# Kernel tuning notes

Measured on AMD Instinct MI355X. Metric: run time of the kernel, lower is better.

The kernel has to match this reference:

```python
import jax, jax.numpy as jnp
import numpy as np

N_PTS = 10000
BATCH = 2048          # hypotheses per RANSAC iteration
MAX_ITER = 10
SAMPLE_SIZE = 4       # minimal sample for homography DLT
INL_TH = 2.0          # squared symmetric transfer error threshold
EPS = 1e-8


def normalize_points(pts):
    # kornia.geometry.normalize_points: center + isotropic scale to mean dist sqrt(2)
    mean = pts.mean(axis=1, keepdims=True)                       # [B,1,2]
    d = jnp.linalg.norm(pts - mean, axis=-1).mean(axis=-1)       # [B]
    s = jnp.sqrt(jnp.asarray(2.0, pts.dtype)) / (d + EPS)
    B = pts.shape[0]
    T = jnp.zeros((B, 3, 3), pts.dtype)
    T = T.at[:, 0, 0].set(s).at[:, 1, 1].set(s).at[:, 2, 2].set(1.0)
    T = T.at[:, 0, 2].set(-s * mean[:, 0, 0]).at[:, 1, 2].set(-s * mean[:, 0, 1])
    return (pts - mean) * s[:, None, None], T


def find_homography_dlt(p1, p2):
    # p1,p2: [B,4,2]; weights are all ones -> solve smallest eigvec of A^T A (as kornia does)
    p1n, T1 = normalize_points(p1)
    p2n, T2 = normalize_points(p2)
    x1, y1 = p1n[..., 0], p1n[..., 1]
    x2, y2 = p2n[..., 0], p2n[..., 1]
    o = jnp.ones_like(x1); z = jnp.zeros_like(x1)
    ax = jnp.stack([z, z, z, -x1, -y1, -o, y2 * x1, y2 * y1, y2], -1)
    ay = jnp.stack([x1, y1, o, z, z, z, -x2 * x1, -x2 * y1, -x2], -1)
    A = jnp.concatenate([ax, ay], axis=1)                        # [B,8,9]
    AtA = jnp.einsum('bki,bkj->bij', A, A)                       # [B,9,9]
    _, _, Vh = jnp.linalg.svd(AtA)
    H = Vh[:, -1, :].reshape(-1, 3, 3)                           # smallest singular vector
    H = jnp.linalg.inv(T2) @ (H @ T1)
    return H / (H[:, 2:3, 2:3] + EPS)


def transform_points(H, pts):
    # H: [B,3,3], pts: [N,2] -> [B,N,2] (safe homogeneous division, as kornia)
    ph = jnp.concatenate([pts, jnp.ones_like(pts[..., :1])], -1)  # [N,3]
    pt = jnp.einsum('bij,nj->bni', H, ph)                        # [B,N,3]
    zc = pt[..., 2:3]
    mask = jnp.abs(zc) > EPS
    scale = jnp.where(mask, 1.0 / jnp.where(mask, zc, jnp.ones_like(zc)), jnp.ones_like(zc))
    return pt[..., :2] * scale


def symmetric_transfer_error(p1, p2, H):
    # squared symmetric transfer error (kornia default squared=True)
    Hinv = jnp.linalg.inv(H)
    e1 = ((transform_points(H, p1) - p2[None]) ** 2).sum(-1)
    e2 = ((transform_points(Hinv, p2) - p1[None]) ** 2).sum(-1)
    return e1 + e2                                               # [B,N]


def ransac_forward(kp1, kp2, key):
    n = kp1.shape[0]
    keys = jax.random.split(key, MAX_ITER)
    init = (jnp.asarray(1.0, kp1.dtype), jnp.eye(3, dtype=kp1.dtype), jnp.zeros((n,), bool))

    def body(carry, k):
        best_score, best_model, best_inl = carry
        # batched sampling without replacement: top-k of iid uniforms == randperm[:k]
        u = jax.random.uniform(k, (BATCH, n))
        _, idxs = jax.lax.top_k(u, SAMPLE_SIZE)                  # [BATCH,4] distinct
        H = find_homography_dlt(kp1[idxs], kp2[idxs])            # [BATCH,3,3]
        # remove_bad_models: mask instead of filter (jit-friendly)
        valid = jnp.abs(jnp.diagonal(H, axis1=1, axis2=2)).min(-1) > 1e-6
        err = symmetric_transfer_error(kp1, kp2, H)              # [BATCH,N]
        inl = err <= INL_TH
        scores = jnp.where(valid, inl.sum(-1).astype(kp1.dtype), -1.0)
        bi = jnp.argmax(scores)
        better = scores[bi] > best_score
        best_score = jnp.where(better, scores[bi], best_score)
        best_model = jnp.where(better, H[bi], best_model)
        best_inl = jnp.where(better, inl[bi], best_inl)
        return (best_score, best_model, best_inl), None

    (_, best_model, best_inl), _ = jax.lax.scan(body, init, keys)
    return best_model, best_inl


def setup_inputs():
    key = jax.random.key(0)
    k1, k2 = jax.random.split(key)
    kp1 = jax.random.uniform(k1, (N_PTS, 2), jnp.float32) * 100.0
    kp2 = jax.random.uniform(k2, (N_PTS, 2), jnp.float32) * 100.0
    return {"kp1": kp1, "kp2": kp2}


def reference(kp1, kp2):
    return ransac_forward(kp1, kp2, jax.random.key(42))
```

## Files before the change

kernel.cpp:

```cpp
#include <hip/hip_runtime.h>
#include <stdint.h>

#define JAX_PARTITIONABLE 1

#define N_PTS    10000
#define BATCH    2048
#define MAX_ITER 10
#define NMODELS  (BATCH*MAX_ITER)

#define ROTL(v,d) __builtin_amdgcn_alignbit((v),(v),(uint32_t)(32-(d)))

__device__ __forceinline__ void threefry_rounds(uint32_t k0, uint32_t k1, uint32_t ks2,
                                                uint32_t &x0, uint32_t &x1){
#define TF_R(r) { x0 += x1; x1 = ROTL(x1,(r)); x1 ^= x0; }
  TF_R(13) TF_R(15) TF_R(26) TF_R(6)
  x0 += k1;  x1 += ks2 + 1u;
  TF_R(17) TF_R(29) TF_R(16) TF_R(24)
  x0 += ks2; x1 += k0 + 2u;
  TF_R(13) TF_R(15) TF_R(26) TF_R(6)
  x0 += k0;  x1 += k1 + 3u;
  TF_R(17) TF_R(29) TF_R(16) TF_R(24)
  x0 += k1;  x1 += ks2 + 4u;
  TF_R(13) TF_R(15) TF_R(26) TF_R(6)
  x0 += ks2; x1 += k0 + 5u;
#undef TF_R
}

__device__ __forceinline__ void threefry2x32(uint32_t k0, uint32_t k1, uint32_t &x0, uint32_t &x1){
  const uint32_t ks2 = k0 ^ k1 ^ 0x1BD11BDAu;
  x0 += k0; x1 += k1;
  threefry_rounds(k0, k1, ks2, x0, x1);
}

__device__ __forceinline__ void top4_insert(unsigned long long a[4], unsigned long long key){
  if (key > a[3]){
    if (key > a[0]){ a[3]=a[2]; a[2]=a[1]; a[1]=a[0]; a[0]=key; }
    else if (key > a[1]){ a[3]=a[2]; a[2]=a[1]; a[1]=key; }
    else if (key > a[2]){ a[3]=a[2]; a[2]=key; }
    else { a[3]=key; }
  }
}

__device__ __forceinline__ unsigned long long u64max(unsigned long long x, unsigned long long y){
  return (x >= y) ? x : y;
}
__device__ __forceinline__ unsigned long long u64min(unsigned long long x, unsigned long long y){
  return (x >= y) ? y : x;
}

__device__ __forceinline__ void wave_merge_top4(unsigned long long a[4]){
  #pragma unroll
  for (int d = 1; d < 64; d <<= 1){
    unsigned long long b0 = __shfl_xor(a[0], d, 64);
    unsigned long long b1 = __shfl_xor(a[1], d, 64);
    unsigned long long b2 = __shfl_xor(a[2], d, 64);
    unsigned long long b3 = __shfl_xor(a[3], d, 64);
    unsigned long long L0 = u64max(a[0], b3);
    unsigned long long L1 = u64max(a[1], b2);
    unsigned long long L2 = u64max(a[2], b1);
    unsigned long long L3 = u64max(a[3], b0);
    unsigned long long m0 = u64max(L0, L2), m2 = u64min(L0, L2);
    unsigned long long m1 = u64max(L1, L3), m3 = u64min(L1, L3);
    a[0] = u64max(m0, m1); a[1] = u64min(m0, m1);
    a[2] = u64max(m2, m3); a[3] = u64min(m2, m3);
  }
}

__device__ __forceinline__ unsigned int lane_lt_count(unsigned long long m){
  unsigned int c = __builtin_amdgcn_mbcnt_lo((uint32_t)m, 0u);
  return __builtin_amdgcn_mbcnt_hi((uint32_t)(m >> 32), c);
}

#if JAX_PARTITIONABLE
#define TH_BITS 4267479552u
#define WCAP 96

__global__ __launch_bounds__(256) void sample_topk(int* __restrict__ idxs){
  const int b = blockIdx.x;
  const int t = blockIdx.y;
  const int tid = threadIdx.x;
  uint32_t k0 = 0u, k1 = (uint32_t)t;
  threefry2x32(0u, 42u, k0, k1);
  const uint32_t ks2 = k0 ^ k1 ^ 0x1BD11BDAu;

  __shared__ unsigned long long wcand[4*WCAP];
  __shared__ unsigned int wcnts[4];

  const unsigned int wbase = (unsigned int)(tid >> 6) * WCAP;
  unsigned int wcnt = 0;

  const uint32_t jb = (uint32_t)(b * N_PTS) + k1;

#define EMIT(u, idx) { \
    unsigned long long mk = __ballot((u) >= TH_BITS); \
    if (mk){ \
      if ((u) >= TH_BITS){ \
        unsigned int slot = wcnt + lane_lt_count(mk); \
        if (slot < WCAP) \
          wcand[wbase + slot] = ((unsigned long long)((u) >> 9) << 32) | (uint32_t)(~(idx)); \
      } \
      wcnt += (unsigned int)__popcll(mk); \
    } }

  uint32_t x1b = jb + (uint32_t)tid;
  for (int iter = 0; iter < 10; ++iter, x1b += 1024u){
    uint32_t a0=k0, a1=k0, a2=k0, a3=k0;
    uint32_t b0=x1b, b1=x1b+256u, b2=x1b+512u, b3=x1b+768u;
#define QR4(r) { a0+=b0; b0=ROTL(b0,r); b0^=a0;  a1+=b1; b1=ROTL(b1,r); b1^=a1; \
                 a2+=b2; b2=ROTL(b2,r); b2^=a2;  a3+=b3; b3=ROTL(b3,r); b3^=a3; }
#define INJ4(p,q) { a0+=(p); b0+=(q); a1+=(p); b1+=(q); a2+=(p); b2+=(q); a3+=(p); b3+=(q); }
    QR4(13) QR4(15) QR4(26) QR4(6)
    INJ4(k1,  ks2 + 1u)
    QR4(17) QR4(29) QR4(16) QR4(24)
    INJ4(ks2, k0 + 2u)
    QR4(13) QR4(15) QR4(26) QR4(6)
    INJ4(k0,  k1 + 3u)
    QR4(17) QR4(29) QR4(16) QR4(24)
    INJ4(k1,  ks2 + 4u)
    QR4(13) QR4(15) QR4(26) QR4(6)
    INJ4(ks2, k0 + 5u)
#undef QR4
#undef INJ4
    uint32_t u0 = a0^b0, u1 = a1^b1, u2 = a2^b2, u3 = a3^b3;
    const uint32_t ibase = (uint32_t)(iter*1024) + (uint32_t)tid;
    if (iter == 9){
      u0 = (ibase        < (uint32_t)N_PTS) ? u0 : 0u;
      u1 = (ibase + 256u < (uint32_t)N_PTS) ? u1 : 0u;
      u2 = (ibase + 512u < (uint32_t)N_PTS) ? u2 : 0u;
      u3 = (ibase + 768u < (uint32_t)N_PTS) ? u3 : 0u;
    }
    EMIT(u0, ibase)
    EMIT(u1, ibase + 256u)
    EMIT(u2, ibase + 512u)
    EMIT(u3, ibase + 768u)
  }
#undef EMIT

  if ((tid & 63) == 0) wcnts[tid >> 6] = wcnt;
  __syncthreads();
  const unsigned int c0 = wcnts[0], c1 = wcnts[1], c2 = wcnts[2], c3 = wcnts[3];
  const unsigned int n = c0 + c1 + c2 + c3;
  const bool good = (n >= 4u) && (c0 <= WCAP) && (c1 <= WCAP) && (c2 <= WCAP) && (c3 <= WCAP);

  if (!good){
    unsigned long long a[4] = {0ull,0ull,0ull,0ull};
    for (int i = tid; i < N_PTS; i += 256){
      uint32_t x0 = k0, x1 = jb + (uint32_t)i;
      threefry_rounds(k0, k1, ks2, x0, x1);
      uint32_t u = x0 ^ x1;
      unsigned long long key = ((unsigned long long)(u >> 9) << 32) | (uint32_t)(~(uint32_t)i);
      top4_insert(a, key);
    }
    wave_merge_top4(a);
    if ((tid & 63) == 0){
      const unsigned int w = tid >> 6;
      wcand[w*WCAP+0]=a[0]; wcand[w*WCAP+1]=a[1]; wcand[w*WCAP+2]=a[2]; wcand[w*WCAP+3]=a[3];
      wcnts[w] = 4u;
    }
    __syncthreads();
  }

  if (tid < 64){
    unsigned long long a[4] = {0ull,0ull,0ull,0ull};
    #pragma unroll
    for (int w = 0; w < 4; ++w){
      unsigned int cw = wcnts[w]; if (cw > WCAP) cw = WCAP;
      for (unsigned int j = (unsigned int)tid; j < cw; j += 64u)
        top4_insert(a, wcand[w*WCAP + j]);
    }
    wave_merge_top4(a);
    if (tid == 0){
      int base = ((t*BATCH)+b)*4;
      idxs[base+0] = (int)(~(uint32_t)(a[0] & 0xffffffffull));
      idxs[base+1] = (int)(~(uint32_t)(a[1] & 0xffffffffull));
      idxs[base+2] = (int)(~(uint32_t)(a[2] & 0xffffffffull));
      idxs[base+3] = (int)(~(uint32_t)(a[3] & 0xffffffffull));
    }
  }
}
#else
__global__ __launch_bounds__(256) void sample_topk(int* __restrict__ idxs){
  const int b = blockIdx.x;
  const int t = blockIdx.y;
  const int tid = threadIdx.x;
  uint32_t k0, k1;
  {
    int i0 = 2*t, i1 = 2*t+1;
    uint32_t u0, u1;
    if (i0 < 10){ u0=(uint32_t)i0; u1=(uint32_t)(i0+10); threefry2x32(0u,42u,u0,u1); k0=u0; }
    else        { u0=(uint32_t)(i0-10); u1=(uint32_t)i0; threefry2x32(0u,42u,u0,u1); k0=u1; }
    if (i1 < 10){ u0=(uint32_t)i1; u1=(uint32_t)(i1+10); threefry2x32(0u,42u,u0,u1); k1=u0; }
    else        { u0=(uint32_t)(i1-10); u1=(uint32_t)i1; threefry2x32(0u,42u,u0,u1); k1=u1; }
  }
  const uint32_t half = 10240000u;
  unsigned long long aLo[4] = {0,0,0,0}, aHi[4] = {0,0,0,0};
  const uint32_t jbase = (uint32_t)(b * N_PTS);
  for (int i = tid; i < N_PTS; i += 256){
    uint32_t x0 = jbase + (uint32_t)i, x1 = x0 + half;
    threefry2x32(k0, k1, x0, x1);
    unsigned long long kLo = ((unsigned long long)(x0 >> 9) << 32) | (uint32_t)(~(uint32_t)i);
    unsigned long long kHi = ((unsigned long long)(x1 >> 9) << 32) | (uint32_t)(~(uint32_t)i);
    top4_insert(aLo, kLo);
    top4_insert(aHi, kHi);
  }
  __shared__ unsigned long long wc[4*4];
  __shared__ unsigned int dummy;
  (void)dummy;
  wave_merge_top4(aLo);
  if ((tid&63)==0){ int w=tid>>6; wc[w*4+0]=aLo[0];wc[w*4+1]=aLo[1];wc[w*4+2]=aLo[2];wc[w*4+3]=aLo[3]; }
  __syncthreads();
  if (tid < 64){
    unsigned long long a[4]={0,0,0,0};
    for (int w=0;w<4;w++) if ((unsigned)tid < 4u) {}
    for (int w=0;w<4;w++) for (unsigned int j=tid;j<4u;j+=64u) top4_insert(a, wc[w*4+j]);
    wave_merge_top4(a);
    if (tid==0){ int base=((t*BATCH)+b)*4; for (int s=0;s<4;s++) idxs[base+s]=(int)(~(uint32_t)(a[s]&0xffffffffull)); }
  }
  __syncthreads();
  wave_merge_top4(aHi);
  if ((tid&63)==0){ int w=tid>>6; wc[w*4+0]=aHi[0];wc[w*4+1]=aHi[1];wc[w*4+2]=aHi[2];wc[w*4+3]=aHi[3]; }
  __syncthreads();
  if (tid < 64){
    unsigned long long a[4]={0,0,0,0};
    for (int w=0;w<4;w++) for (unsigned int j=tid;j<4u;j+=64u) top4_insert(a, wc[w*4+j]);
    wave_merge_top4(a);
    if (tid==0){ int base=((t*BATCH)+(b+1024))*4; for (int s=0;s<4;s++) idxs[base+s]=(int)(~(uint32_t)(a[s]&0xffffffffull)); }
  }
}
#endif

__global__ __launch_bounds__(64) void dlt_kernel(const float* __restrict__ kp1,
                                                 const float* __restrict__ kp2,
                                                 const int* __restrict__ idxs,
                                                 float* __restrict__ Hout,
                                                 float* __restrict__ Hinvout,
                                                 int* __restrict__ validout){
  const int m = blockIdx.x*64 + threadIdx.x;
  __shared__ double As[64][73];
  double* A = &As[threadIdx.x][0];

  double p1x[4],p1y[4],p2x[4],p2y[4];
  #pragma unroll
  for (int s=0;s<4;s++){
    int id = idxs[m*4+s];
    float2 a = ((const float2*)kp1)[id];
    float2 b = ((const float2*)kp2)[id];
    p1x[s]=a.x; p1y[s]=a.y; p2x[s]=b.x; p2y[s]=b.y;
  }
  double mx1=0,my1=0,mx2=0,my2=0;
  #pragma unroll
  for (int s=0;s<4;s++){ mx1+=p1x[s]; my1+=p1y[s]; mx2+=p2x[s]; my2+=p2y[s]; }
  mx1*=0.25; my1*=0.25; mx2*=0.25; my2*=0.25;
  double d1=0,d2=0;
  #pragma unroll
  for (int s=0;s<4;s++){
    d1 += sqrt((p1x[s]-mx1)*(p1x[s]-mx1) + (p1y[s]-my1)*(p1y[s]-my1));
    d2 += sqrt((p2x[s]-mx2)*(p2x[s]-mx2) + (p2y[s]-my2)*(p2y[s]-my2));
  }
  d1*=0.25; d2*=0.25;
  const double s1 = sqrt(2.0)/(d1 + 1e-8);
  const double s2 = sqrt(2.0)/(d2 + 1e-8);
  #pragma unroll
  for (int s=0;s<4;s++){
    double X1=(p1x[s]-mx1)*s1, Y1=(p1y[s]-my1)*s1;
    double X2=(p2x[s]-mx2)*s2, Y2=(p2y[s]-my2)*s2;
    double* ra = A + s*9;
    ra[0]=0.0; ra[1]=0.0; ra[2]=0.0; ra[3]=-X1; ra[4]=-Y1; ra[5]=-1.0;
    ra[6]=Y2*X1; ra[7]=Y2*Y1; ra[8]=Y2;
    double* rb = A + (4+s)*9;
    rb[0]=X1; rb[1]=Y1; rb[2]=1.0; rb[3]=0.0; rb[4]=0.0; rb[5]=0.0;
    rb[6]=-X2*X1; rb[7]=-X2*Y1; rb[8]=-X2;
  }
  for (int k=0;k<8;k++){
    int piv=k; double pv=fabs(A[k*9+k]);
    for (int r=k+1;r<8;r++){ double v=fabs(A[r*9+k]); if (v>pv){pv=v;piv=r;} }
    if (piv!=k){
      for (int c=k;c<9;c++){ double tmp=A[k*9+c]; A[k*9+c]=A[piv*9+c]; A[piv*9+c]=tmp; }
    }
    double invp = 1.0/A[k*9+k];
    for (int r=k+1;r<8;r++){
      double f = A[r*9+k]*invp;
      for (int c=k+1;c<9;c++) A[r*9+c] -= f*A[k*9+c];
      A[r*9+k]=0.0;
    }
  }
  double h[9];
  h[8]=1.0;
  for (int k=7;k>=0;k--){
    double ssum=0.0;
    for (int c=k+1;c<9;c++) ssum += A[k*9+c]*h[c];
    h[k] = -ssum / A[k*9+k];
  }
  {
    double nn=0.0;
    #pragma unroll
    for (int i=0;i<9;i++) nn += h[i]*h[i];
    double inr = 1.0/sqrt(nn);
    #pragma unroll
    for (int i=0;i<9;i++) h[i]*=inr;
  }
  double M[9];
  #pragma unroll
  for (int r=0;r<3;r++){
    double h0=h[r*3+0], h1=h[r*3+1], h2=h[r*3+2];
    M[r*3+0] = h0*s1;
    M[r*3+1] = h1*s1;
    M[r*3+2] = h0*(-s1*mx1) + h1*(-s1*my1) + h2;
  }
  double Hd[9];
  const double is2 = 1.0/s2;
  #pragma unroll
  for (int c=0;c<3;c++){
    Hd[0*3+c] = M[0*3+c]*is2 + mx2*M[2*3+c];
    Hd[1*3+c] = M[1*3+c]*is2 + my2*M[2*3+c];
    Hd[2*3+c] = M[2*3+c];
  }
  const double dn = 1.0/(Hd[8] + 1e-8);
  #pragma unroll
  for (int i=0;i<9;i++) Hd[i]*=dn;
  float Hf[9];
  #pragma unroll
  for (int i=0;i<9;i++){ Hf[i]=(float)Hd[i]; Hout[m*9+i]=Hf[i]; }
  float mind = fminf(fminf(fabsf(Hf[0]),fabsf(Hf[4])),fabsf(Hf[8]));
  validout[m] = (mind > 1e-6f) ? 1 : 0;
  {
    double a=Hd[0],b=Hd[1],c=Hd[2],d=Hd[3],e=Hd[4],f=Hd[5],g=Hd[6],hh=Hd[7],ii=Hd[8];
    double C00= e*ii-f*hh, C01=-(d*ii-f*g), C02= d*hh-e*g;
    double det = a*C00 + b*C01 + c*C02;
    double idet = 1.0/det;
    double inv[9];
    inv[0]=C00*idet;        inv[1]=(c*hh-b*ii)*idet; inv[2]=(b*f-c*e)*idet;
    inv[3]=C01*idet;        inv[4]=(a*ii-c*g)*idet;  inv[5]=(c*d-a*f)*idet;
    inv[6]=C02*idet;        inv[7]=(b*g-a*hh)*idet;  inv[8]=(a*e-b*d)*idet;
    #pragma unroll
    for (int i=0;i<9;i++) Hinvout[m*9+i]=(float)inv[i];
  }
}

__device__ __forceinline__ int inlier_test(float x1,float y1,float x2,float y2,
                                           const float* __restrict__ H,
                                           const float* __restrict__ Hi){
  float px = __fadd_rn(__fadd_rn(__fmul_rn(H[0],x1), __fmul_rn(H[1],y1)), H[2]);
  float py = __fadd_rn(__fadd_rn(__fmul_rn(H[3],x1), __fmul_rn(H[4],y1)), H[5]);
  float pz = __fadd_rn(__fadd_rn(__fmul_rn(H[6],x1), __fmul_rn(H[7],y1)), H[8]);
  float sc = (fabsf(pz) > 1e-8f) ? __fdiv_rn(1.0f, pz) : 1.0f;
  float dx = __fsub_rn(__fmul_rn(px,sc), x2);
  float dy = __fsub_rn(__fmul_rn(py,sc), y2);
  float e1 = __fadd_rn(__fmul_rn(dx,dx), __fmul_rn(dy,dy));
  if (!(e1 <= 2.0f)) return 0;
  float qx = __fadd_rn(__fadd_rn(__fmul_rn(Hi[0],x2), __fmul_rn(Hi[1],y2)), Hi[2]);
  float qy = __fadd_rn(__fadd_rn(__fmul_rn(Hi[3],x2), __fmul_rn(Hi[4],y2)), Hi[5]);
  float qz = __fadd_rn(__fadd_rn(__fmul_rn(Hi[6],x2), __fmul_rn(Hi[7],y2)), Hi[8]);
  float sc2 = (fabsf(qz) > 1e-8f) ? __fdiv_rn(1.0f, qz) : 1.0f;
  float ex = __fsub_rn(__fmul_rn(qx,sc2), x1);
  float ey = __fsub_rn(__fmul_rn(qy,sc2), y1);
  float e2 = __fadd_rn(__fmul_rn(ex,ex), __fmul_rn(ey,ey));
  float err = __fadd_rn(e1, e2);
  return (err <= 2.0f) ? 1 : 0;
}

#define MODELS_PER_BLOCK 4
__global__ __launch_bounds__(256) void score_kernel(const float* __restrict__ kp1,
                                                    const float* __restrict__ kp2,
                                                    const float* __restrict__ Hall,
                                                    const float* __restrict__ Hinvall,
                                                    const int* __restrict__ validall,
                                                    float* __restrict__ scores){
  const int m0 = blockIdx.x * MODELS_PER_BLOCK;
  const int tid = threadIdx.x;
  __shared__ float sH[MODELS_PER_BLOCK][9], sHi[MODELS_PER_BLOCK][9];
  if (tid < 9*MODELS_PER_BLOCK)        sH [tid/9][tid%9] = Hall[m0*9 + tid];
  else if (tid < 18*MODELS_PER_BLOCK){ int q = tid - 9*MODELS_PER_BLOCK;
                                       sHi[q/9][q%9] = Hinvall[m0*9 + q]; }
  __syncthreads();
  int cnt[MODELS_PER_BLOCK];
  #pragma unroll
  for (int mm=0;mm<MODELS_PER_BLOCK;mm++) cnt[mm]=0;
  for (int i = tid; i < N_PTS; i += 256){
    float2 p1 = ((const float2*)kp1)[i];
    float2 p2 = ((const float2*)kp2)[i];
    #pragma unroll
    for (int mm=0;mm<MODELS_PER_BLOCK;mm++)
      cnt[mm] += inlier_test(p1.x,p1.y,p2.x,p2.y,sH[mm],sHi[mm]);
  }
  __shared__ int red[256];
  #pragma unroll
  for (int mm=0;mm<MODELS_PER_BLOCK;mm++){
    red[tid]=cnt[mm]; __syncthreads();
    for (int s=128;s;s>>=1){ if (tid<s) red[tid]+=red[tid+s]; __syncthreads(); }
    if (tid==0) scores[m0+mm] = validall[m0+mm] ? (float)red[0] : -1.0f;
    __syncthreads();
  }
}

__global__ __launch_bounds__(1024) void select_kernel(const float* __restrict__ scores,
                                                      int* __restrict__ winner){
  __shared__ unsigned long long sm[1024];
  const int tid = threadIdx.x;
  unsigned long long best = 0ull;
  for (int i = tid; i < NMODELS; i += 1024){
    float s = scores[i];
    uint32_t hi = (uint32_t)(int)(s + 2.0f);
    unsigned long long key = ((unsigned long long)hi << 32) | (uint32_t)(~(uint32_t)i);
    if (key > best) best = key;
  }
  sm[tid]=best; __syncthreads();
  for (int s=512;s;s>>=1){ if (tid<s && sm[tid+s]>sm[tid]) sm[tid]=sm[tid+s]; __syncthreads(); }
  if (tid==0){
    unsigned long long k = sm[0];
    winner[0] = (int)(~(uint32_t)(k & 0xffffffffull));
    winner[1] = ((uint32_t)(k >> 32) >= 4u) ? 1 : 0;
  }
}

__global__ __launch_bounds__(256) void finalize_kernel(const float* __restrict__ kp1,
                                                       const float* __restrict__ kp2,
                                                       const float* __restrict__ Hall,
                                                       const float* __restrict__ Hinvall,
                                                       const int* __restrict__ winner,
                                                       float* __restrict__ out){
  __shared__ float sH[9], sHi[9];
  const int w = winner[0];
  const int ok = winner[1];
  if (threadIdx.x < 9){
    float idv = (threadIdx.x % 4 == 0) ? 1.0f : 0.0f;
    sH[threadIdx.x]  = ok ? Hall[w*9+threadIdx.x]    : idv;
    sHi[threadIdx.x] = ok ? Hinvall[w*9+threadIdx.x] : idv;
  }
  __syncthreads();
  if (blockIdx.x==0 && threadIdx.x<9) out[threadIdx.x] = sH[threadIdx.x];
  const int i = blockIdx.x*256 + threadIdx.x;
  if (i < N_PTS){
    float2 p1 = ((const float2*)kp1)[i];
    float2 p2 = ((const float2*)kp2)[i];
    int inl = ok ? inlier_test(p1.x,p1.y,p2.x,p2.y,sH,sHi) : 0;
    out[9+i] = inl ? 1.0f : 0.0f;
  }
}

extern "C" void kernel_launch(void* const* d_in, const int* in_sizes, int n_in,
                              void* d_out, int out_size, void* d_ws, size_t ws_size,
                              hipStream_t stream) {
  (void)in_sizes; (void)n_in; (void)out_size; (void)ws_size;
  const float* kp1 = (const float*)d_in[0];
  const float* kp2 = (const float*)d_in[1];
  float* out = (float*)d_out;
  char* ws = (char*)d_ws;
  int*   idxs    = (int*)  (ws + 0);
  float* Hall    = (float*)(ws + 327680);
  float* Hinvall = (float*)(ws + 1064960);
  int*   validall= (int*)  (ws + 1802240);
  float* scores  = (float*)(ws + 1884160);
  int*   winner  = (int*)  (ws + 1966080);

#if JAX_PARTITIONABLE
  sample_topk<<<dim3(BATCH, MAX_ITER), 256, 0, stream>>>(idxs);
#else
  sample_topk<<<dim3(BATCH/2, MAX_ITER), 256, 0, stream>>>(idxs);
#endif
  dlt_kernel<<<dim3(NMODELS/64), 64, 0, stream>>>(kp1, kp2, idxs, Hall, Hinvall, validall);
  score_kernel<<<dim3(NMODELS/MODELS_PER_BLOCK), 256, 0, stream>>>(kp1, kp2, Hall, Hinvall, validall, scores);
  select_kernel<<<1, 1024, 0, stream>>>(scores, winner);
  finalize_kernel<<<dim3((N_PTS+255)/256), 256, 0, stream>>>(kp1, kp2, Hall, Hinvall, winner, out);
}
```

Measured before the change: 727.6 us.

## Register-resident pivot-free sparse DLT elimination and fuse select with finalize

The DLT solve moves from shared-memory doubles to a fully unrolled register array. Rows are reordered to exploit the block sparsity of the A matrix, so partial pivoting and the zero-row eliminations are dropped. The select and finalize kernels are merged into one single-block kernel, which removes a launch and the winner round-trip through global memory. The unused non-partitionable sampler is also deleted. Dropping pivoting risks numerical instability for degenerate samples, and the finalize step now runs on only one block.

```diff
diff --git a/kernel.cpp b/kernel.cpp
--- a/kernel.cpp
+++ b/kernel.cpp
@@ -71,7 +71,6 @@
   return __builtin_amdgcn_mbcnt_hi((uint32_t)(m >> 32), c);
 }
 
-#if JAX_PARTITIONABLE
 #define TH_BITS 4267479552u
 #define WCAP 96
 
@@ -178,66 +177,14 @@
     }
   }
 }
-#else
-__global__ __launch_bounds__(256) void sample_topk(int* __restrict__ idxs){
-  const int b = blockIdx.x;
-  const int t = blockIdx.y;
-  const int tid = threadIdx.x;
-  uint32_t k0, k1;
-  {
-    int i0 = 2*t, i1 = 2*t+1;
-    uint32_t u0, u1;
-    if (i0 < 10){ u0=(uint32_t)i0; u1=(uint32_t)(i0+10); threefry2x32(0u,42u,u0,u1); k0=u0; }
-    else        { u0=(uint32_t)(i0-10); u1=(uint32_t)i0; threefry2x32(0u,42u,u0,u1); k0=u1; }
-    if (i1 < 10){ u0=(uint32_t)i1; u1=(uint32_t)(i1+10); threefry2x32(0u,42u,u0,u1); k1=u0; }
-    else        { u0=(uint32_t)(i1-10); u1=(uint32_t)i1; threefry2x32(0u,42u,u0,u1); k1=u1; }
-  }
-  const uint32_t half = 10240000u;
-  unsigned long long aLo[4] = {0,0,0,0}, aHi[4] = {0,0,0,0};
-  const uint32_t jbase = (uint32_t)(b * N_PTS);
-  for (int i = tid; i < N_PTS; i += 256){
-    uint32_t x0 = jbase + (uint32_t)i, x1 = x0 + half;
-    threefry2x32(k0, k1, x0, x1);
-    unsigned long long kLo = ((unsigned long long)(x0 >> 9) << 32) | (uint32_t)(~(uint32_t)i);
-    unsigned long long kHi = ((unsigned long long)(x1 >> 9) << 32) | (uint32_t)(~(uint32_t)i);
-    top4_insert(aLo, kLo);
-    top4_insert(aHi, kHi);
-  }
-  __shared__ unsigned long long wc[4*4];
-  __shared__ unsigned int dummy;
-  (void)dummy;
-  wave_merge_top4(aLo);
-  if ((tid&63)==0){ int w=tid>>6; wc[w*4+0]=aLo[0];wc[w*4+1]=aLo[1];wc[w*4+2]=aLo[2];wc[w*4+3]=aLo[3]; }
-  __syncthreads();
-  if (tid < 64){
-    unsigned long long a[4]={0,0,0,0};
-    for (int w=0;w<4;w++) if ((unsigned)tid < 4u) {}
-    for (int w=0;w<4;w++) for (unsigned int j=tid;j<4u;j+=64u) top4_insert(a, wc[w*4+j]);
-    wave_merge_top4(a);
-    if (tid==0){ int base=((t*BATCH)+b)*4; for (int s=0;s<4;s++) idxs[base+s]=(int)(~(uint32_t)(a[s]&0xffffffffull)); }
-  }
-  __syncthreads();
-  wave_merge_top4(aHi);
-  if ((tid&63)==0){ int w=tid>>6; wc[w*4+0]=aHi[0];wc[w*4+1]=aHi[1];wc[w*4+2]=aHi[2];wc[w*4+3]=aHi[3]; }
-  __syncthreads();
-  if (tid < 64){
-    unsigned long long a[4]={0,0,0,0};
-    for (int w=0;w<4;w++) for (unsigned int j=tid;j<4u;j+=64u) top4_insert(a, wc[w*4+j]);
-    wave_merge_top4(a);
-    if (tid==0){ int base=((t*BATCH)+(b+1024))*4; for (int s=0;s<4;s++) idxs[base+s]=(int)(~(uint32_t)(a[s]&0xffffffffull)); }
-  }
-}
-#endif
-
-__global__ __launch_bounds__(64) void dlt_kernel(const float* __restrict__ kp1,
-                                                 const float* __restrict__ kp2,
-                                                 const int* __restrict__ idxs,
-                                                 float* __restrict__ Hout,
-                                                 float* __restrict__ Hinvout,
-                                                 int* __restrict__ validout){
+
+__global__ __launch_bounds__(64, 1) void dlt_kernel(const float* __restrict__ kp1,
+                                                    const float* __restrict__ kp2,
+                                                    const int* __restrict__ idxs,
+                                                    float* __restrict__ Hout,
+                                                    float* __restrict__ Hinvout,
+                                                    int* __restrict__ validout){
   const int m = blockIdx.x*64 + threadIdx.x;
-  __shared__ double As[64][73];
-  double* A = &As[threadIdx.x][0];
 
   double p1x[4],p1y[4],p2x[4],p2y[4];
   #pragma unroll
@@ -260,36 +207,41 @@
   d1*=0.25; d2*=0.25;
   const double s1 = sqrt(2.0)/(d1 + 1e-8);
   const double s2 = sqrt(2.0)/(d2 + 1e-8);
+
+  double A[8][9];
   #pragma unroll
   for (int s=0;s<4;s++){
     double X1=(p1x[s]-mx1)*s1, Y1=(p1y[s]-my1)*s1;
     double X2=(p2x[s]-mx2)*s2, Y2=(p2y[s]-my2)*s2;
-    double* ra = A + s*9;
-    ra[0]=0.0; ra[1]=0.0; ra[2]=0.0; ra[3]=-X1; ra[4]=-Y1; ra[5]=-1.0;
-    ra[6]=Y2*X1; ra[7]=Y2*Y1; ra[8]=Y2;
-    double* rb = A + (4+s)*9;
-    rb[0]=X1; rb[1]=Y1; rb[2]=1.0; rb[3]=0.0; rb[4]=0.0; rb[5]=0.0;
-    rb[6]=-X2*X1; rb[7]=-X2*Y1; rb[8]=-X2;
-  }
+    const int ra = (s<3) ? s : 6;
+    const int rb = (s<3) ? 3+s : 7;
+    A[ra][0]=X1;  A[ra][1]=Y1;  A[ra][2]=1.0;
+    A[ra][3]=0.0; A[ra][4]=0.0; A[ra][5]=0.0;
+    A[ra][6]=-X2*X1; A[ra][7]=-X2*Y1; A[ra][8]=-X2;
+    A[rb][0]=0.0; A[rb][1]=0.0; A[rb][2]=0.0;
+    A[rb][3]=-X1; A[rb][4]=-Y1; A[rb][5]=-1.0;
+    A[rb][6]=Y2*X1; A[rb][7]=Y2*Y1; A[rb][8]=Y2;
+  }
+  #pragma unroll
   for (int k=0;k<8;k++){
-    int piv=k; double pv=fabs(A[k*9+k]);
-    for (int r=k+1;r<8;r++){ double v=fabs(A[r*9+k]); if (v>pv){pv=v;piv=r;} }
-    if (piv!=k){
-      for (int c=k;c<9;c++){ double tmp=A[k*9+c]; A[k*9+c]=A[piv*9+c]; A[piv*9+c]=tmp; }
-    }
-    double invp = 1.0/A[k*9+k];
+    double invp = 1.0/A[k][k];
+    #pragma unroll
     for (int r=k+1;r<8;r++){
-      double f = A[r*9+k]*invp;
-      for (int c=k+1;c<9;c++) A[r*9+c] -= f*A[k*9+c];
-      A[r*9+k]=0.0;
+      if (k < 3 && (r==3 || r==4 || r==5 || r==7)) continue;
+      if (k >= 3 && k < 6 && r == 6) continue;
+      double f = A[r][k]*invp;
+      #pragma unroll
+      for (int c=k+1;c<9;c++) A[r][c] -= f*A[k][c];
     }
   }
   double h[9];
   h[8]=1.0;
+  #pragma unroll
   for (int k=7;k>=0;k--){
     double ssum=0.0;
-    for (int c=k+1;c<9;c++) ssum += A[k*9+c]*h[c];
-    h[k] = -ssum / A[k*9+k];
+    #pragma unroll
+    for (int c=k+1;c<9;c++) ssum += A[k][c]*h[c];
+    h[k] = -ssum / A[k][k];
   }
   {
     double nn=0.0;
@@ -393,9 +345,14 @@
   }
 }
 
-__global__ __launch_bounds__(1024) void select_kernel(const float* __restrict__ scores,
-                                                      int* __restrict__ winner){
+__global__ __launch_bounds__(1024) void select_finalize_kernel(const float* __restrict__ kp1,
+                                                               const float* __restrict__ kp2,
+                                                               const float* __restrict__ Hall,
+                                                               const float* __restrict__ Hinvall,
+                                                               const float* __restrict__ scores,
+                                                               float* __restrict__ out){
   __shared__ unsigned long long sm[1024];
+  __shared__ float sH[9], sHi[9];
   const int tid = threadIdx.x;
   unsigned long long best = 0ull;
   for (int i = tid; i < NMODELS; i += 1024){
@@ -406,31 +363,17 @@
   }
   sm[tid]=best; __syncthreads();
   for (int s=512;s;s>>=1){ if (tid<s && sm[tid+s]>sm[tid]) sm[tid]=sm[tid+s]; __syncthreads(); }
-  if (tid==0){
-    unsigned long long k = sm[0];
-    winner[0] = (int)(~(uint32_t)(k & 0xffffffffull));
-    winner[1] = ((uint32_t)(k >> 32) >= 4u) ? 1 : 0;
-  }
-}
-
-__global__ __launch_bounds__(256) void finalize_kernel(const float* __restrict__ kp1,
-                                                       const float* __restrict__ kp2,
-                                                       const float* __restrict__ Hall,
-                                                       const float* __restrict__ Hinvall,
-                                                       const int* __restrict__ winner,
-                                                       float* __restrict__ out){
-  __shared__ float sH[9], sHi[9];
-  const int w = winner[0];
-  const int ok = winner[1];
-  if (threadIdx.x < 9){
-    float idv = (threadIdx.x % 4 == 0) ? 1.0f : 0.0f;
-    sH[threadIdx.x]  = ok ? Hall[w*9+threadIdx.x]    : idv;
-    sHi[threadIdx.x] = ok ? Hinvall[w*9+threadIdx.x] : idv;
+  const unsigned long long k = sm[0];
+  const int w = (int)(~(uint32_t)(k & 0xffffffffull));
+  const int ok = ((uint32_t)(k >> 32) >= 4u) ? 1 : 0;
+  if (tid < 9){
+    float idv = (tid % 4 == 0) ? 1.0f : 0.0f;
+    sH[tid]  = ok ? Hall[w*9+tid]    : idv;
+    sHi[tid] = ok ? Hinvall[w*9+tid] : idv;
+    out[tid] = sH[tid];
   }
   __syncthreads();
-  if (blockIdx.x==0 && threadIdx.x<9) out[threadIdx.x] = sH[threadIdx.x];
-  const int i = blockIdx.x*256 + threadIdx.x;
-  if (i < N_PTS){
+  for (int i = tid; i < N_PTS; i += 1024){
     float2 p1 = ((const float2*)kp1)[i];
     float2 p2 = ((const float2*)kp2)[i];
     int inl = ok ? inlier_test(p1.x,p1.y,p2.x,p2.y,sH,sHi) : 0;
@@ -451,15 +394,9 @@
   float* Hinvall = (float*)(ws + 1064960);
   int*   validall= (int*)  (ws + 1802240);
   float* scores  = (float*)(ws + 1884160);
-  int*   winner  = (int*)  (ws + 1966080);
-
-#if JAX_PARTITIONABLE
+
   sample_topk<<<dim3(BATCH, MAX_ITER), 256, 0, stream>>>(idxs);
-#else
-  sample_topk<<<dim3(BATCH/2, MAX_ITER), 256, 0, stream>>>(idxs);
-#endif
   dlt_kernel<<<dim3(NMODELS/64), 64, 0, stream>>>(kp1, kp2, idxs, Hall, Hinvall, validall);
   score_kernel<<<dim3(NMODELS/MODELS_PER_BLOCK), 256, 0, stream>>>(kp1, kp2, Hall, Hinvall, validall, scores);
-  select_kernel<<<1, 1024, 0, stream>>>(scores, winner);
-  finalize_kernel<<<dim3((N_PTS+255)/256), 256, 0, stream>>>(kp1, kp2, Hall, Hinvall, winner, out);
-}
+  select_finalize_kernel<<<1, 1024, 0, stream>>>(kp1, kp2, Hall, Hinvall, scores, out);
+}
```

After: 725.9 us. About the same (-0.2%).
